# Kernel tuning notes

Hardware: AMD Instinct MI355X
Metric: run time of the kernel (lower is better)

The kernel has to match this reference:

```python
import jax, jax.numpy as jnp
import numpy as np

# Canonical DAG: L topological levels of N nodes each; every node in level l>0
# has K predecessors in level l-1, each edge carrying a scalar weight.
# Input nodes (level 0) take x columns directly (no activation), matching the
# torch module. Output = activations of the (sorted) last-level nodes.

B, N, K, L = 1024, 5000, 16, 10  # batch, nodes/level, fan-in, levels
NEG_SLOPE = 0.1                  # LeakyReLU(0.1) as in the module


def setup_inputs() -> dict:
    key = jax.random.key(0)
    k_x, k_s, k_w, k_b = jax.random.split(key, 4)
    x = jax.random.normal(k_x, (B, N), dtype=jnp.float32)
    # predecessor indices into the previous level, per level 1..L-1
    src_idx = jax.random.randint(k_s, (L - 1, N, K), 0, N)
    # scalar edge weights and node biases ~ N(0, 0.1), as in __init__
    weights = jax.random.normal(k_w, (L - 1, N, K), dtype=jnp.float32) * 0.1
    biases = jax.random.normal(k_b, (L - 1, N), dtype=jnp.float32) * 0.1
    return {"x": x, "src_idx": src_idx, "weights": weights, "biases": biases}


def reference(x, src_idx, weights, biases):
    b, n = x.shape
    k = src_idx.shape[-1]

    def level(act, params):
        s, w, bias = params  # s,w: [N,K], bias: [N]
        # gather predecessor activations: [B, N, K]
        gathered = jnp.take(act, s.reshape(-1), axis=1).reshape(b, n, k)
        # weighted sum over predecessors + bias, then LeakyReLU(0.1)
        pre = jnp.einsum('bnk,nk->bn', gathered, w) + bias
        return jax.nn.leaky_relu(pre, NEG_SLOPE), None

    out, _ = jax.lax.scan(level, x, (src_idx, weights, biases))
    return out  # [B, N] activations of output nodes (sorted order)
```

## Files before the change

### kernel.cpp

```cpp
#include <hip/hip_runtime.h>


#define TB 1024
#define TN 5000
#define TK 16
#define TLV 9
#define CPG 4
#define NG  (TB / CPG)
#define LT  1024
#define NPANEL ((TN + 63) / 64)
#define PEL (NPANEL * TK * 64)

typedef unsigned int u32;
typedef unsigned short u16;
typedef _Float16 h2 __attribute__((ext_vector_type(2)));

__device__ __forceinline__ h2 u2h(u32 v) { return __builtin_bit_cast(h2, v); }
__device__ __forceinline__ u32 h2u(h2 h) { return __builtin_bit_cast(u32, h); }
__device__ __forceinline__ u32 packf(float a, float b) {
    h2 h; h.x = (_Float16)a; h.y = (_Float16)b;
    return h2u(h);
}

__global__ __launch_bounds__(256) void k_pack(
    const int* __restrict__ idx, const float* __restrict__ w,
    u32* __restrict__ pe)
{
    const int j = blockIdx.x * 256 + threadIdx.x;
    if (j < TLV * TN * TK) {
        const int l = j / (TN * TK);
        const int r = j % (TN * TK);
        const int n = r / TK;
        const int k = r % TK;
        h2 hw; hw.x = (_Float16)w[j]; hw.y = (_Float16)0.0f;
        const u32 v = ((u32)idx[j] & 0xffffu) | (h2u(hw) << 16);
        pe[(size_t)l * PEL + (n >> 6) * (TK * 64) + k * 64 + (n & 63)] = v;
    }
}

__global__ __launch_bounds__(LT) void k_fused(
    const float* __restrict__ x,
    float* __restrict__ out,
    const u32* __restrict__ pe,
    const float* __restrict__ biases)
{
    __shared__ uint2 buf[2][TN];
    const int g = blockIdx.x;
    const int t = threadIdx.x;

    {
        const float* xp0 = x + (size_t)(g * CPG + 0) * TN;
        const float* xp1 = x + (size_t)(g * CPG + 1) * TN;
        const float* xp2 = x + (size_t)(g * CPG + 2) * TN;
        const float* xp3 = x + (size_t)(g * CPG + 3) * TN;
        for (int n = t; n < TN; n += LT) {
            uint2 v;
            v.x = packf(xp0[n], xp1[n]);
            v.y = packf(xp2[n], xp3[n]);
            buf[0][n] = v;
        }
    }
    __syncthreads();

    int cur = 0;
    for (int l = 0; l < TLV; ++l) {
        const u32*   ep_l = pe + (size_t)l * PEL;
        const float* b_l  = biases + (size_t)l * TN;
        for (int n = t; n < TN; n += LT) {
            const u32* ep = ep_l + (n >> 6) * (TK * 64) + (n & 63);
            const float bvf = b_l[n];
            h2 bb; bb.x = (_Float16)bvf; bb.y = (_Float16)bvf;
            h2 a01 = bb, a23 = bb;

            #pragma unroll
            for (int k = 0; k < TK; ++k) {
                const u32 e = ep[k * 64];
                const u32 s = e & 0xffffu;
                const h2 w2 = u2h(__builtin_amdgcn_perm(e, e, 0x03020302u));
                const uint2 av = buf[cur][s];
                a01 = w2 * u2h(av.x) + a01;
                a23 = w2 * u2h(av.y) + a23;
            }

            h2 tenth; tenth.x = (_Float16)0.1f; tenth.y = (_Float16)0.1f;
            a01 = __builtin_elementwise_max(a01, a01 * tenth);
            a23 = __builtin_elementwise_max(a23, a23 * tenth);

            uint2 r; r.x = h2u(a01); r.y = h2u(a23);
            buf[cur ^ 1][n] = r;
        }
        __syncthreads();
        cur ^= 1;
    }

    {
        float* op0 = out + (size_t)(g * CPG + 0) * TN;
        float* op1 = out + (size_t)(g * CPG + 1) * TN;
        float* op2 = out + (size_t)(g * CPG + 2) * TN;
        float* op3 = out + (size_t)(g * CPG + 3) * TN;
        for (int n = t; n < TN; n += LT) {
            const uint2 v = buf[cur][n];
            h2 h;
            h = u2h(v.x); op0[n] = (float)h.x; op1[n] = (float)h.y;
            h = u2h(v.y); op2[n] = (float)h.x; op3[n] = (float)h.y;
        }
    }
}

extern "C" void kernel_launch(void* const* d_in, const int* in_sizes, int n_in,
                              void* d_out, int out_size, void* d_ws, size_t ws_size,
                              hipStream_t stream)
{
    const float* x       = (const float*)d_in[0];
    const int*   src_idx = (const int*)  d_in[1];
    const float* weights = (const float*)d_in[2];
    const float* biases  = (const float*)d_in[3];
    float* out = (float*)d_out;

    u32* pe = (u32*)d_ws;

    {
        const int ne = TLV * TN * TK;
        hipLaunchKernelGGL(k_pack, dim3((ne + 255) / 256), dim3(256), 0, stream,
                           src_idx, weights, pe);
    }
    hipLaunchKernelGGL(k_fused, dim3(NG), dim3(LT), 0, stream,
                       x, out, pe, biases);
}
```

Before: 128.3 us.

## Sort and rotate edges by LDS bank and prescale indices to byte offsets

The pack kernel now has one wave handle one 64-node panel. Each lane sorts its 16 edges by the low 4 bits of the source index, then rotates them by lane id. The goal is that lanes in a wave hit different LDS bank groups on each gather step, which cuts bank conflicts in the fused kernel's inner loop. Source indices are also stored pre-multiplied by 8 as byte offsets, which removes an address shift per gather. The costs are a heavier pack kernel, whose selection sort on a dynamically indexed register array may spill to scratch, and a changed fp16 accumulation order.

```diff
diff --git a/kernel.cpp b/kernel.cpp
--- a/kernel.cpp
+++ b/kernel.cpp
@@ -26,16 +26,38 @@
     const int* __restrict__ idx, const float* __restrict__ w,
     u32* __restrict__ pe)
 {
-    const int j = blockIdx.x * 256 + threadIdx.x;
-    if (j < TLV * TN * TK) {
-        const int l = j / (TN * TK);
-        const int r = j % (TN * TK);
-        const int n = r / TK;
-        const int k = r % TK;
-        h2 hw; hw.x = (_Float16)w[j]; hw.y = (_Float16)0.0f;
-        const u32 v = ((u32)idx[j] & 0xffffu) | (h2u(hw) << 16);
-        pe[(size_t)l * PEL + (n >> 6) * (TK * 64) + k * 64 + (n & 63)] = v;
+    const int wid  = (blockIdx.x * 256 + threadIdx.x) >> 6;
+    const int lane = threadIdx.x & 63;
+    const int l = wid / NPANEL;
+    const int p = wid % NPANEL;
+    if (l >= TLV) return;
+    const int n = p * 64 + lane;
+
+    u32 ev[TK];
+    if (n < TN) {
+        const size_t base = ((size_t)l * TN + n) * TK;
+        #pragma unroll
+        for (int k = 0; k < TK; ++k) {
+            const u32 s = (u32)idx[base + k];
+            h2 hw; hw.x = (_Float16)w[base + k]; hw.y = (_Float16)0.0f;
+            ev[k] = (s * 8u) | (h2u(hw) << 16);
+        }
+    } else {
+        #pragma unroll
+        for (int k = 0; k < TK; ++k) ev[k] = 0;
     }
+
+    for (int i = 0; i < TK - 1; ++i) {
+        int m = i;
+        for (int j = i + 1; j < TK; ++j)
+            if (((ev[j] >> 3) & 15u) < ((ev[m] >> 3) & 15u)) m = j;
+        u32 t = ev[i]; ev[i] = ev[m]; ev[m] = t;
+    }
+
+    const u32 rot = (u32)(lane & 15);
+    u32* dst = pe + (size_t)l * PEL + (size_t)p * (TK * 64) + lane;
+    for (int k = 0; k < TK; ++k)
+        dst[k * 64] = ev[(k + rot) & 15u];
 }
 
 __global__ __launch_bounds__(LT) void k_fused(
@@ -66,6 +88,7 @@
     for (int l = 0; l < TLV; ++l) {
         const u32*   ep_l = pe + (size_t)l * PEL;
         const float* b_l  = biases + (size_t)l * TN;
+        const char*  base = reinterpret_cast<const char*>(buf[cur]);
         for (int n = t; n < TN; n += LT) {
             const u32* ep = ep_l + (n >> 6) * (TK * 64) + (n & 63);
             const float bvf = b_l[n];
@@ -74,10 +97,10 @@
 
             #pragma unroll
             for (int k = 0; k < TK; ++k) {
-                const u32 e = ep[k * 64];
-                const u32 s = e & 0xffffu;
+                const u32 e  = ep[k * 64];
+                const u32 s8 = e & 0xffffu;
                 const h2 w2 = u2h(__builtin_amdgcn_perm(e, e, 0x03020302u));
-                const uint2 av = buf[cur][s];
+                const uint2 av = *reinterpret_cast<const uint2*>(base + s8);
                 a01 = w2 * u2h(av.x) + a01;
                 a23 = w2 * u2h(av.y) + a23;
             }
@@ -120,8 +143,9 @@
     u32* pe = (u32*)d_ws;
 
     {
-        const int ne = TLV * TN * TK;
-        hipLaunchKernelGGL(k_pack, dim3((ne + 255) / 256), dim3(256), 0, stream,
+        const int nwaves  = TLV * NPANEL;
+        const int nblocks = (nwaves + 3) / 4;
+        hipLaunchKernelGGL(k_pack, dim3(nblocks), dim3(256), 0, stream,
                            src_idx, weights, pe);
     }
     hipLaunchKernelGGL(k_fused, dim3(NG), dim3(LT), 0, stream,
```

New measurement: 146.6 us. +14.3%, slower.
